# Kernel optimization log

Measured on AMD Instinct MI355X. Metric: run time of the kernel, lower is better.

Reference implementation:

```python
import jax, jax.numpy as jnp
import numpy as np

B, T, N, D = 64, 12, 512, 2      # batch, seq_len, num_nodes, input_dim
R, M, O, H = 64, 64, 1, 12       # rnn_units, message_size, output_dim, horizon


def setup_inputs() -> dict:
    key = jax.random.key(0)
    ks = jax.random.split(key, 12)
    inputs = jax.random.normal(ks[0], (B, T, N, D), jnp.float32)
    h0 = jax.random.normal(ks[1], (N, B, R), jnp.float32)  # torch.randn initial state
    adj = jax.random.uniform(ks[2], (N, N), jnp.float32)
    mask = jax.random.uniform(ks[3], (N, N)) < 0.05
    adj = jnp.where(mask, adj, 0.0)
    s = 1.0 / np.sqrt(R)
    u = lambda k, shape: jax.random.uniform(k, shape, jnp.float32, -s, s)
    return {
        "inputs": inputs, "h0": h0, "adj": adj,
        "W_msg": u(ks[4], (M, R)), "b_msg": u(ks[5], (M,)),
        "W_ih": u(ks[6], (3 * R, D + M)), "W_hh": u(ks[7], (3 * R, R)),
        "b_ih": u(ks[8], (3 * R,)), "b_hh": u(ks[9], (3 * R,)),
        "W_out": u(ks[10], (O * H, R)), "b_out": u(ks[11], (O * H,)),
    }


def reference(inputs, h0, adj, W_msg, b_msg, W_ih, W_hh, b_ih, b_hh, W_out, b_out):
    # mask matches the 'adj[j,i] > 0' guard in the python double loop
    adj_pos = jnp.where(adj > 0.0, adj, 0.0)

    def step(h, x_t):
        # h: [N, B, R]; x_t: [B, N, D]
        hw = h @ W_msg.T + b_msg                       # M_t(h): [N, B, M]
        # m[i] = sum_j adj[j, i] * hw[j]  -> dense masked aggregation
        m = jnp.einsum('ji,jbm->ibm', adj_pos, hw)     # [N, B, M]
        inp2 = jnp.concatenate([m, jnp.transpose(x_t, (1, 0, 2))], axis=2)  # [N, B, M+D]
        # torch GRUCell math (elementwise over the N*B 'batch'):
        gi = inp2 @ W_ih.T + b_ih                      # [N, B, 3R]
        gh = h @ W_hh.T + b_hh                         # [N, B, 3R]
        i_r, i_z, i_n = jnp.split(gi, 3, axis=-1)
        h_r, h_z, h_n = jnp.split(gh, 3, axis=-1)
        r = jax.nn.sigmoid(i_r + h_r)
        z = jax.nn.sigmoid(i_z + h_z)
        n = jnp.tanh(i_n + r * h_n)
        h_new = (1.0 - z) * n + z * h
        return h_new, None

    xs = jnp.transpose(inputs, (1, 0, 2, 3))           # [T, B, N, D]
    h, _ = jax.lax.scan(step, h0, xs)                  # [N, B, R]
    out = h @ W_out.T + b_out                          # R_t(h): [N, B, O*H]
    out = out.reshape(N, B, H, O)                      # reshape(N, B, horizon, -1)
    return jnp.transpose(out, (1, 2, 0, 3))            # [B, H, N, O]
```

## Files before the change

### kernel.cpp

```cpp
#include <hip/hip_runtime.h>

#define Bb 64
#define Tt 12
#define Nn 512
#define Dd 2
#define G3 192
#define Hh 12
#define CSR_CAP 96

typedef float f32x4 __attribute__((ext_vector_type(4)));
typedef _Float16 f16;
typedef _Float16 f16x8 __attribute__((ext_vector_type(8)));
typedef unsigned int uint_t;

__device__ __forceinline__ int swz4(int row, int bo) {
  return row * 256 + (bo ^ ((row & 7) << 4));
}

__global__ __launch_bounds__(256) void init_kernel(
    const float* __restrict__ h0, const float* __restrict__ adj,
    const float* __restrict__ W_msg, const float* __restrict__ W_ih,
    const float* __restrict__ W_hh, const float* __restrict__ b_ih,
    const float* __restrict__ b_hh, const float* __restrict__ b_msg,
    float* __restrict__ h_ws, f16* __restrict__ g_w, f16* __restrict__ g_wlo,
    float* __restrict__ g_f, int* __restrict__ g_cj,
    float* __restrict__ g_ca, int* __restrict__ g_nnz) {
  __shared__ int s_wavecnt[4];
  const int n = blockIdx.x, tid = threadIdx.x, l = tid & 63, wt = tid >> 6;

  {
    const int j0 = tid * 2, j1 = j0 + 1;
    const float a0 = adj[j0 * Nn + n];
    const float a1 = adj[j1 * Nn + n];
    unsigned long long mk0 = __ballot(a0 > 0.f);
    unsigned long long mk1 = __ballot(a1 > 0.f);
    if (l == 0) s_wavecnt[wt] = __popcll(mk0) + __popcll(mk1);
    __syncthreads();
    int base = 0;
#pragma unroll
    for (int w = 0; w < 4; ++w)
      if (w < wt) base += s_wavecnt[w];
    unsigned long long lt = (1ull << l) - 1ull;
    int pos = base + __popcll(mk0 & lt) + __popcll(mk1 & lt);
    if (a0 > 0.f) {
      if (pos < CSR_CAP) { g_cj[n * CSR_CAP + pos] = j0; g_ca[n * CSR_CAP + pos] = a0; }
      ++pos;
    }
    if (a1 > 0.f && pos < CSR_CAP) { g_cj[n * CSR_CAP + pos] = j1; g_ca[n * CSR_CAP + pos] = a1; }
    if (tid == 0) {
      int tot = s_wavecnt[0] + s_wavecnt[1] + s_wavecnt[2] + s_wavecnt[3];
      g_nnz[n] = tot < CSR_CAP ? tot : CSR_CAP;
    }
  }

  if (n == 0) {
    for (int tile = wt; tile < 24; tile += 4) {
      const int nt = tile >> 1, kt = tile & 1;
      const int wrow = nt * 16 + (l & 15);
      const int kc = kt * 32 + ((l >> 4) << 3);
      const float* s2 = W_ih + wrow * 66 + kc;
      const float* s1 = W_hh + wrow * 64 + kc;
#pragma unroll
      for (int j = 0; j < 8; ++j) {
        const float w2 = s2[j];
        const f16 h2 = (f16)w2;
        g_w[tile * 512 + l * 8 + j] = h2;
        g_wlo[tile * 512 + l * 8 + j] = (f16)(w2 - (float)h2);
        const float w1 = s1[j];
        const f16 h1 = (f16)w1;
        g_w[12288 + tile * 512 + l * 8 + j] = h1;
        g_wlo[12288 + tile * 512 + l * 8 + j] = (f16)(w1 - (float)h1);
      }
    }
    for (int tile = wt; tile < 8; tile += 4) {
      const int nt = tile >> 1, kt = tile & 1;
      const int wrow = nt * 16 + (l & 15);
      const int kc = kt * 32 + ((l >> 4) << 3);
      const float* s1 = W_msg + wrow * 64 + kc;
#pragma unroll
      for (int j = 0; j < 8; ++j) g_w[24576 + tile * 512 + l * 8 + j] = (f16)s1[j];
    }
    if (tid < G3) {
      g_f[tid * 2] = W_ih[tid * 66 + 64];
      g_f[tid * 2 + 1] = W_ih[tid * 66 + 65];
      g_f[384 + tid] = b_ih[tid];
      g_f[576 + tid] = b_hh[tid];
    }
    if (tid < 64) g_f[768 + tid] = b_msg[tid];
  }

  const float4* src = (const float4*)(h0 + ((size_t)n << 12));
  float4* dst = (float4*)(h_ws + ((size_t)n << 12));
  for (int i = tid; i < 1024; i += 256) dst[i] = src[i];
}

__global__ __launch_bounds__(256) void hw0_kernel(
    const float* __restrict__ h0, const f16* __restrict__ g_w,
    const float* __restrict__ g_f, f16* __restrict__ hw_out) {
  __shared__ float h_lds[4096];
  const int n = blockIdx.x, tid = threadIdx.x, l = tid & 63, wt = tid >> 6;
  {
    const int row = tid >> 2, c0 = (tid & 3) << 4;
    const float4* src = (const float4*)(h0 + ((n << 6) + row) * 64 + c0);
#pragma unroll
    for (int q = 0; q < 4; ++q)
      *(float4*)((char*)h_lds + swz4(row, c0 * 4 + q * 16)) = src[q];
  }
  const int ar = wt * 16 + (l & 15);
  const int bo = (l >> 4) << 5;
  float4 p0 = *(const float4*)((const char*)h_lds + swz4(ar, bo));
  float4 p1 = *(const float4*)((const char*)h_lds + swz4(ar, bo + 16));
  float4 p2 = *(const float4*)((const char*)h_lds + swz4(ar, 128 + bo));
  float4 p3 = *(const float4*)((const char*)h_lds + swz4(ar, 128 + bo + 16));
  f16x8 ahi0, alo0, ahi1, alo1;
  {
    float v[16] = {p0.x, p0.y, p0.z, p0.w, p1.x, p1.y, p1.z, p1.w,
                   p2.x, p2.y, p2.z, p2.w, p3.x, p3.y, p3.z, p3.w};
#pragma unroll
    for (int j = 0; j < 8; ++j) {
      f16 h = (f16)v[j];          ahi0[j] = h; alo0[j] = (f16)(v[j] - (float)h);
      f16 g = (f16)v[8 + j];      ahi1[j] = g; alo1[j] = (f16)(v[8 + j] - (float)g);
    }
  }
#pragma unroll
  for (int nt = 0; nt < 4; ++nt) {
    const f16x8 b0 = *(const f16x8*)(g_w + 24576 + (nt * 2 + 0) * 512 + l * 8);
    const f16x8 b1 = *(const f16x8*)(g_w + 24576 + (nt * 2 + 1) * 512 + l * 8);
    f32x4 c = {0.f, 0.f, 0.f, 0.f};
    c = __builtin_amdgcn_mfma_f32_16x16x32_f16(ahi0, b0, c, 0, 0, 0);
    c = __builtin_amdgcn_mfma_f32_16x16x32_f16(alo0, b0, c, 0, 0, 0);
    c = __builtin_amdgcn_mfma_f32_16x16x32_f16(ahi1, b1, c, 0, 0, 0);
    c = __builtin_amdgcn_mfma_f32_16x16x32_f16(alo1, b1, c, 0, 0, 0);
    const int col = nt * 16 + (l & 15);
    const float bm = g_f[768 + col];
#pragma unroll
    for (int g = 0; g < 4; ++g) {
      const int row = wt * 16 + ((l >> 4) << 2) + g;
      hw_out[((n << 6) + row) * 64 + col] = (f16)(c[g] + bm);
    }
  }
}

__global__ __launch_bounds__(256, 2) void step_kernel(
    const float* __restrict__ xin, float* __restrict__ h_ws,
    const uint4* __restrict__ g_blob, const f16* __restrict__ g_wlo,
    const int* __restrict__ g_cj, const float* __restrict__ g_ca,
    const int* __restrict__ g_nnz, const f16* __restrict__ hw_rd,
    f16* __restrict__ hw_wr, int t) {
  __shared__ uint4 sBlob[3792];
  __shared__ float h_lds[4096];
  __shared__ int s_cj[CSR_CAP];
  __shared__ float s_ca[CSR_CAP];
  const f16* sBih = (const f16*)sBlob;
  const f16* sBhh = sBih + 12288;
  const f16* sBmsg = sBih + 24576;
  const float* sF = (const float*)(sBih + 28672);
  const float* sWx = sF;
  const float* s_bih = sF + 384;
  const float* s_bhh = sF + 576;
  const float* s_bmsg = sF + 768;

  const int n = blockIdx.x, tid = threadIdx.x, l = tid & 63, wt = tid >> 6;

  for (int i = tid; i < 3792; i += 256) sBlob[i] = g_blob[i];
  if (tid < CSR_CAP) {
    s_cj[tid] = g_cj[n * CSR_CAP + tid];
    s_ca[tid] = g_ca[n * CSR_CAP + tid];
  }
  const int nnz = g_nnz[n];

  {
    const int row = tid >> 2, c0 = (tid & 3) << 4;
    const float4* src = (const float4*)(h_ws + ((n << 6) + row) * 64 + c0);
#pragma unroll
    for (int q = 0; q < 4; ++q)
      *(float4*)((char*)h_lds + swz4(row, c0 * 4 + q * 16)) = src[q];
  }
  float hreg[4][4];
#pragma unroll
  for (int ct = 0; ct < 4; ++ct)
#pragma unroll
    for (int g = 0; g < 4; ++g) {
      const int row = wt * 16 + ((l >> 4) << 2) + g;
      hreg[ct][g] = h_ws[((n << 6) + row) * 64 + ct * 16 + (l & 15)];
    }
  __syncthreads();

  const int mb = wt * 16 + (l & 15);
  const int mc0 = (l >> 4) << 3;
  float accm[16];
#pragma unroll
  for (int e = 0; e < 16; ++e) accm[e] = 0.f;
  for (int k = 0; k < nnz; ++k) {
    const int j = s_cj[k];
    const float a = s_ca[k];
    const f16* base = hw_rd + ((j << 6) + mb) * 64 + mc0;
    const f16x8 v0 = *(const f16x8*)(base);
    const f16x8 v1 = *(const f16x8*)(base + 32);
#pragma unroll
    for (int jj = 0; jj < 8; ++jj) {
      accm[jj] += a * (float)v0[jj];
      accm[8 + jj] += a * (float)v1[jj];
    }
  }
  f16x8 mhi0, mlo0, mhi1, mlo1;
#pragma unroll
  for (int jj = 0; jj < 8; ++jj) {
    f16 h = (f16)accm[jj];       mhi0[jj] = h; mlo0[jj] = (f16)(accm[jj] - (float)h);
    f16 g = (f16)accm[8 + jj];   mhi1[jj] = g; mlo1[jj] = (f16)(accm[8 + jj] - (float)g);
  }

  const int ar = wt * 16 + (l & 15);
  const int bo = (l >> 4) << 5;
  f16x8 ahi0, alo0, ahi1, alo1;
  {
    float4 p0 = *(const float4*)((const char*)h_lds + swz4(ar, bo));
    float4 p1 = *(const float4*)((const char*)h_lds + swz4(ar, bo + 16));
    float4 p2 = *(const float4*)((const char*)h_lds + swz4(ar, 128 + bo));
    float4 p3 = *(const float4*)((const char*)h_lds + swz4(ar, 128 + bo + 16));
    float v[16] = {p0.x, p0.y, p0.z, p0.w, p1.x, p1.y, p1.z, p1.w,
                   p2.x, p2.y, p2.z, p2.w, p3.x, p3.y, p3.z, p3.w};
#pragma unroll
    for (int j = 0; j < 8; ++j) {
      f16 h = (f16)v[j];        ahi0[j] = h; alo0[j] = (f16)(v[j] - (float)h);
      f16 g = (f16)v[8 + j];    ahi1[j] = g; alo1[j] = (f16)(v[8 + j] - (float)g);
    }
  }

  f32x4 cgi[12], cgh[12];
#pragma unroll
  for (int nt = 0; nt < 12; ++nt) {
    cgi[nt] = {0.f, 0.f, 0.f, 0.f};
    cgh[nt] = {0.f, 0.f, 0.f, 0.f};
  }
#pragma unroll
  for (int nt = 0; nt < 12; ++nt) {
    const f16x8 bh0 = *(const f16x8*)(sBhh + (nt * 2 + 0) * 512 + l * 8);
    const f16x8 bh1 = *(const f16x8*)(sBhh + (nt * 2 + 1) * 512 + l * 8);
    const f16x8 bhL0 = *(const f16x8*)(g_wlo + 12288 + (nt * 2 + 0) * 512 + l * 8);
    const f16x8 bhL1 = *(const f16x8*)(g_wlo + 12288 + (nt * 2 + 1) * 512 + l * 8);
    cgh[nt] = __builtin_amdgcn_mfma_f32_16x16x32_f16(ahi0, bh0, cgh[nt], 0, 0, 0);
    cgh[nt] = __builtin_amdgcn_mfma_f32_16x16x32_f16(alo0, bh0, cgh[nt], 0, 0, 0);
    cgh[nt] = __builtin_amdgcn_mfma_f32_16x16x32_f16(ahi1, bh1, cgh[nt], 0, 0, 0);
    cgh[nt] = __builtin_amdgcn_mfma_f32_16x16x32_f16(alo1, bh1, cgh[nt], 0, 0, 0);
    cgh[nt] = __builtin_amdgcn_mfma_f32_16x16x32_f16(ahi0, bhL0, cgh[nt], 0, 0, 0);
    cgh[nt] = __builtin_amdgcn_mfma_f32_16x16x32_f16(ahi1, bhL1, cgh[nt], 0, 0, 0);
    const f16x8 bi0 = *(const f16x8*)(sBih + (nt * 2 + 0) * 512 + l * 8);
    const f16x8 bi1 = *(const f16x8*)(sBih + (nt * 2 + 1) * 512 + l * 8);
    const f16x8 biL0 = *(const f16x8*)(g_wlo + (nt * 2 + 0) * 512 + l * 8);
    const f16x8 biL1 = *(const f16x8*)(g_wlo + (nt * 2 + 1) * 512 + l * 8);
    cgi[nt] = __builtin_amdgcn_mfma_f32_16x16x32_f16(mhi0, bi0, cgi[nt], 0, 0, 0);
    cgi[nt] = __builtin_amdgcn_mfma_f32_16x16x32_f16(mlo0, bi0, cgi[nt], 0, 0, 0);
    cgi[nt] = __builtin_amdgcn_mfma_f32_16x16x32_f16(mhi1, bi1, cgi[nt], 0, 0, 0);
    cgi[nt] = __builtin_amdgcn_mfma_f32_16x16x32_f16(mlo1, bi1, cgi[nt], 0, 0, 0);
    cgi[nt] = __builtin_amdgcn_mfma_f32_16x16x32_f16(mhi0, biL0, cgi[nt], 0, 0, 0);
    cgi[nt] = __builtin_amdgcn_mfma_f32_16x16x32_f16(mhi1, biL1, cgi[nt], 0, 0, 0);
  }

  float x0[4], x1[4];
#pragma unroll
  for (int g = 0; g < 4; ++g) {
    const int brow = wt * 16 + ((l >> 4) << 2) + g;
    const float* xp = xin + ((brow * Tt + t) * Nn + n) * Dd;
    x0[g] = xp[0];
    x1[g] = xp[1];
  }
#pragma unroll
  for (int ct = 0; ct < 4; ++ct) {
    const int colr = ct * 16 + (l & 15);
    const float wr0 = sWx[colr * 2], wr1 = sWx[colr * 2 + 1];
    const float wz0 = sWx[(colr + 64) * 2], wz1 = sWx[(colr + 64) * 2 + 1];
    const float wn0 = sWx[(colr + 128) * 2], wn1 = sWx[(colr + 128) * 2 + 1];
    const float bir = s_bih[colr], biz = s_bih[colr + 64], bin_ = s_bih[colr + 128];
    const float bhr = s_bhh[colr], bhz = s_bhh[colr + 64], bhn = s_bhh[colr + 128];
#pragma unroll
    for (int g = 0; g < 4; ++g) {
      const int row = wt * 16 + ((l >> 4) << 2) + g;
      const float gir = cgi[ct][g] + x0[g] * wr0 + x1[g] * wr1 + bir;
      const float giz = cgi[ct + 4][g] + x0[g] * wz0 + x1[g] * wz1 + biz;
      const float gin = cgi[ct + 8][g] + x0[g] * wn0 + x1[g] * wn1 + bin_;
      const float ghr = cgh[ct][g] + bhr;
      const float ghz = cgh[ct + 4][g] + bhz;
      const float ghn = cgh[ct + 8][g] + bhn;
      const float rg = 1.f / (1.f + __expf(-(gir + ghr)));
      const float zg = 1.f / (1.f + __expf(-(giz + ghz)));
      const float pa = gin + rg * ghn;
      const float e2 = __expf(-2.f * fabsf(pa));
      float th = (1.f - e2) / (1.f + e2);
      th = copysignf(th, pa);
      const float hn = (1.f - zg) * th + zg * hreg[ct][g];
      h_ws[((n << 6) + row) * 64 + colr] = hn;
      *(float*)((char*)h_lds + swz4(row, colr * 4)) = hn;
    }
  }

  if (t < Tt - 1) {
    f16x8 nhi0, nlo0, nhi1, nlo1;
    {
      float4 p0 = *(const float4*)((const char*)h_lds + swz4(ar, bo));
      float4 p1 = *(const float4*)((const char*)h_lds + swz4(ar, bo + 16));
      float4 p2 = *(const float4*)((const char*)h_lds + swz4(ar, 128 + bo));
      float4 p3 = *(const float4*)((const char*)h_lds + swz4(ar, 128 + bo + 16));
      float v[16] = {p0.x, p0.y, p0.z, p0.w, p1.x, p1.y, p1.z, p1.w,
                     p2.x, p2.y, p2.z, p2.w, p3.x, p3.y, p3.z, p3.w};
#pragma unroll
      for (int j = 0; j < 8; ++j) {
        f16 h = (f16)v[j];        nhi0[j] = h; nlo0[j] = (f16)(v[j] - (float)h);
        f16 g = (f16)v[8 + j];    nhi1[j] = g; nlo1[j] = (f16)(v[8 + j] - (float)g);
      }
    }
#pragma unroll
    for (int nt = 0; nt < 4; ++nt) {
      const f16x8 b0 = *(const f16x8*)(sBmsg + (nt * 2 + 0) * 512 + l * 8);
      const f16x8 b1 = *(const f16x8*)(sBmsg + (nt * 2 + 1) * 512 + l * 8);
      f32x4 c = {0.f, 0.f, 0.f, 0.f};
      c = __builtin_amdgcn_mfma_f32_16x16x32_f16(nhi0, b0, c, 0, 0, 0);
      c = __builtin_amdgcn_mfma_f32_16x16x32_f16(nlo0, b0, c, 0, 0, 0);
      c = __builtin_amdgcn_mfma_f32_16x16x32_f16(nhi1, b1, c, 0, 0, 0);
      c = __builtin_amdgcn_mfma_f32_16x16x32_f16(nlo1, b1, c, 0, 0, 0);
      const int col = nt * 16 + (l & 15);
      const float bm = s_bmsg[col];
#pragma unroll
      for (int g = 0; g < 4; ++g) {
        const int row = wt * 16 + ((l >> 4) << 2) + g;
        hw_wr[((n << 6) + row) * 64 + col] = (f16)(c[g] + bm);
      }
    }
  }
}

__global__ __launch_bounds__(256) void out_kernel(
    const float* __restrict__ h_ws, const float* __restrict__ W_out,
    const float* __restrict__ b_out, float* __restrict__ out) {
  __shared__ float sWo[Hh * 64];
  __shared__ float sbo[Hh];
  const int n = blockIdx.x, tid = threadIdx.x;
  for (int i = tid; i < Hh * 64; i += 256) sWo[i] = W_out[i];
  if (tid < Hh) sbo[tid] = b_out[tid];
  __syncthreads();
  for (int q = tid; q < Bb * Hh; q += 256) {
    const int b = q / Hh;
    const int o = q - b * Hh;
    const float* hr = h_ws + ((n << 6) + b) * 64;
    const float* wr = sWo + o * 64;
    float acc = sbo[o];
#pragma unroll 8
    for (int k = 0; k < 64; ++k) acc += hr[k] * wr[k];
    out[(b * Hh + o) * Nn + n] = acc;
  }
}

extern "C" void kernel_launch(void* const* d_in, const int* in_sizes, int n_in,
                              void* d_out, int out_size, void* d_ws, size_t ws_size,
                              hipStream_t stream) {
  const float* xin = (const float*)d_in[0];
  const float* h0 = (const float*)d_in[1];
  const float* adj = (const float*)d_in[2];
  const float* W_msg = (const float*)d_in[3];
  const float* b_msg = (const float*)d_in[4];
  const float* W_ih = (const float*)d_in[5];
  const float* W_hh = (const float*)d_in[6];
  const float* b_ih = (const float*)d_in[7];
  const float* b_hh = (const float*)d_in[8];
  const float* W_out = (const float*)d_in[9];
  const float* b_out = (const float*)d_in[10];
  float* out = (float*)d_out;

  char* ws = (char*)d_ws;
  float* h_ws = (float*)ws;
  f16* hwA = (f16*)(ws + (8u << 20));
  f16* hwB = (f16*)(ws + (12u << 20));
  char* base16 = ws + (16u << 20);
  f16* g_w = (f16*)base16;
  float* g_f = (float*)(base16 + 57344);
  f16* g_wlo = (f16*)(base16 + 61440);
  int* g_cj = (int*)(base16 + 110592);
  float* g_ca = (float*)(base16 + 110592 + 196608);
  int* g_nnz = (int*)(base16 + 110592 + 393216);
  const uint4* g_blob = (const uint4*)g_w;

  init_kernel<<<Nn, 256, 0, stream>>>(h0, adj, W_msg, W_ih, W_hh, b_ih, b_hh,
                                      b_msg, h_ws, g_w, g_wlo, g_f, g_cj, g_ca,
                                      g_nnz);
  hw0_kernel<<<Nn, 256, 0, stream>>>(h0, g_w, g_f, hwA);
  for (int t = 0; t < Tt; ++t) {
    f16* rd = (t & 1) ? hwB : hwA;
    f16* wr = (t & 1) ? hwA : hwB;
    step_kernel<<<Nn, 256, 0, stream>>>(xin, h_ws, g_blob, g_wlo, g_cj, g_ca,
                                        g_nnz, rd, wr, t);
  }
  out_kernel<<<Nn, 256, 0, stream>>>(h_ws, W_out, b_out, out);
}
```

Before: 469.7 us.

## Fuse output projection into last step, drop weight lo-splits, store hw in fp32

Several changes at once. The lo-part correction MFMAs on the GRU weights are removed, roughly halving matrix work per step. The message buffer hw moves from fp16 to fp32 and the gather is unrolled by two with float4 loads. The first step reads h0 directly instead of copying it, and the output projection is folded into the final step with an MFMA, which removes one launch. It also moves the CSR reads out of LDS and zero-pads the CSR. The risks are lower GRU-weight precision and twice the gather traffic from fp32 hw.

```diff
diff --git a/kernel.cpp b/kernel.cpp
--- a/kernel.cpp
+++ b/kernel.cpp
@@ -11,22 +11,25 @@
 typedef float f32x4 __attribute__((ext_vector_type(4)));
 typedef _Float16 f16;
 typedef _Float16 f16x8 __attribute__((ext_vector_type(8)));
-typedef unsigned int uint_t;
 
 __device__ __forceinline__ int swz4(int row, int bo) {
   return row * 256 + (bo ^ ((row & 7) << 4));
 }
 
 __global__ __launch_bounds__(256) void init_kernel(
-    const float* __restrict__ h0, const float* __restrict__ adj,
-    const float* __restrict__ W_msg, const float* __restrict__ W_ih,
-    const float* __restrict__ W_hh, const float* __restrict__ b_ih,
-    const float* __restrict__ b_hh, const float* __restrict__ b_msg,
-    float* __restrict__ h_ws, f16* __restrict__ g_w, f16* __restrict__ g_wlo,
+    const float* __restrict__ adj, const float* __restrict__ W_msg,
+    const float* __restrict__ W_ih, const float* __restrict__ W_hh,
+    const float* __restrict__ b_ih, const float* __restrict__ b_hh,
+    const float* __restrict__ b_msg, f16* __restrict__ g_w,
     float* __restrict__ g_f, int* __restrict__ g_cj,
     float* __restrict__ g_ca, int* __restrict__ g_nnz) {
   __shared__ int s_wavecnt[4];
   const int n = blockIdx.x, tid = threadIdx.x, l = tid & 63, wt = tid >> 6;
+
+  if (tid < CSR_CAP) {
+    g_cj[n * CSR_CAP + tid] = 0;
+    g_ca[n * CSR_CAP + tid] = 0.f;
+  }
 
   {
     const int j0 = tid * 2, j1 = j0 + 1;
@@ -62,14 +65,8 @@
       const float* s1 = W_hh + wrow * 64 + kc;
 #pragma unroll
       for (int j = 0; j < 8; ++j) {
-        const float w2 = s2[j];
-        const f16 h2 = (f16)w2;
-        g_w[tile * 512 + l * 8 + j] = h2;
-        g_wlo[tile * 512 + l * 8 + j] = (f16)(w2 - (float)h2);
-        const float w1 = s1[j];
-        const f16 h1 = (f16)w1;
-        g_w[12288 + tile * 512 + l * 8 + j] = h1;
-        g_wlo[12288 + tile * 512 + l * 8 + j] = (f16)(w1 - (float)h1);
+        g_w[tile * 512 + l * 8 + j] = (f16)s2[j];
+        g_w[12288 + tile * 512 + l * 8 + j] = (f16)s1[j];
       }
     }
     for (int tile = wt; tile < 8; tile += 4) {
@@ -88,15 +85,11 @@
     }
     if (tid < 64) g_f[768 + tid] = b_msg[tid];
   }
-
-  const float4* src = (const float4*)(h0 + ((size_t)n << 12));
-  float4* dst = (float4*)(h_ws + ((size_t)n << 12));
-  for (int i = tid; i < 1024; i += 256) dst[i] = src[i];
 }
 
 __global__ __launch_bounds__(256) void hw0_kernel(
     const float* __restrict__ h0, const f16* __restrict__ g_w,
-    const float* __restrict__ g_f, f16* __restrict__ hw_out) {
+    const float* __restrict__ g_f, float* __restrict__ hw_out) {
   __shared__ float h_lds[4096];
   const int n = blockIdx.x, tid = threadIdx.x, l = tid & 63, wt = tid >> 6;
   {
@@ -108,18 +101,18 @@
   }
   const int ar = wt * 16 + (l & 15);
   const int bo = (l >> 4) << 5;
-  float4 p0 = *(const float4*)((const char*)h_lds + swz4(ar, bo));
-  float4 p1 = *(const float4*)((const char*)h_lds + swz4(ar, bo + 16));
-  float4 p2 = *(const float4*)((const char*)h_lds + swz4(ar, 128 + bo));
-  float4 p3 = *(const float4*)((const char*)h_lds + swz4(ar, 128 + bo + 16));
   f16x8 ahi0, alo0, ahi1, alo1;
   {
+    float4 p0 = *(const float4*)((const char*)h_lds + swz4(ar, bo));
+    float4 p1 = *(const float4*)((const char*)h_lds + swz4(ar, bo + 16));
+    float4 p2 = *(const float4*)((const char*)h_lds + swz4(ar, 128 + bo));
+    float4 p3 = *(const float4*)((const char*)h_lds + swz4(ar, 128 + bo + 16));
     float v[16] = {p0.x, p0.y, p0.z, p0.w, p1.x, p1.y, p1.z, p1.w,
                    p2.x, p2.y, p2.z, p2.w, p3.x, p3.y, p3.z, p3.w};
 #pragma unroll
     for (int j = 0; j < 8; ++j) {
-      f16 h = (f16)v[j];          ahi0[j] = h; alo0[j] = (f16)(v[j] - (float)h);
-      f16 g = (f16)v[8 + j];      ahi1[j] = g; alo1[j] = (f16)(v[8 + j] - (float)g);
+      f16 h = (f16)v[j];        ahi0[j] = h; alo0[j] = (f16)(v[j] - (float)h);
+      f16 g = (f16)v[8 + j];    ahi1[j] = g; alo1[j] = (f16)(v[8 + j] - (float)g);
     }
   }
 #pragma unroll
@@ -136,21 +129,20 @@
 #pragma unroll
     for (int g = 0; g < 4; ++g) {
       const int row = wt * 16 + ((l >> 4) << 2) + g;
-      hw_out[((n << 6) + row) * 64 + col] = (f16)(c[g] + bm);
+      hw_out[((n << 6) + row) * 64 + col] = c[g] + bm;
     }
   }
 }
 
 __global__ __launch_bounds__(256, 2) void step_kernel(
-    const float* __restrict__ xin, float* __restrict__ h_ws,
-    const uint4* __restrict__ g_blob, const f16* __restrict__ g_wlo,
+    const float* __restrict__ xin, const float* __restrict__ h_src,
+    float* __restrict__ h_ws, const uint4* __restrict__ g_blob,
     const int* __restrict__ g_cj, const float* __restrict__ g_ca,
-    const int* __restrict__ g_nnz, const f16* __restrict__ hw_rd,
-    f16* __restrict__ hw_wr, int t) {
-  __shared__ uint4 sBlob[3792];
+    const int* __restrict__ g_nnz, const float* __restrict__ hw_rd,
+    float* __restrict__ hw_wr, const float* __restrict__ W_out,
+    const float* __restrict__ b_out, float* __restrict__ out, int t) {
+  __shared__ uint4 sBlob[3840];
   __shared__ float h_lds[4096];
-  __shared__ int s_cj[CSR_CAP];
-  __shared__ float s_ca[CSR_CAP];
   const f16* sBih = (const f16*)sBlob;
   const f16* sBhh = sBih + 12288;
   const f16* sBmsg = sBih + 24576;
@@ -162,53 +154,61 @@
 
   const int n = blockIdx.x, tid = threadIdx.x, l = tid & 63, wt = tid >> 6;
 
-  for (int i = tid; i < 3792; i += 256) sBlob[i] = g_blob[i];
-  if (tid < CSR_CAP) {
-    s_cj[tid] = g_cj[n * CSR_CAP + tid];
-    s_ca[tid] = g_ca[n * CSR_CAP + tid];
-  }
-  const int nnz = g_nnz[n];
-
+  float x0[4], x1[4];
+#pragma unroll
+  for (int g = 0; g < 4; ++g) {
+    const int brow = wt * 16 + ((l >> 4) << 2) + g;
+    const float2 xv = *(const float2*)(xin + ((brow * Tt + t) * Nn + n) * Dd);
+    x0[g] = xv.x; x1[g] = xv.y;
+  }
+  float hreg[4][4];
+#pragma unroll
+  for (int ct = 0; ct < 4; ++ct)
+#pragma unroll
+    for (int g = 0; g < 4; ++g) {
+      const int row = wt * 16 + ((l >> 4) << 2) + g;
+      hreg[ct][g] = h_src[((n << 6) + row) * 64 + ct * 16 + (l & 15)];
+    }
   {
     const int row = tid >> 2, c0 = (tid & 3) << 4;
-    const float4* src = (const float4*)(h_ws + ((n << 6) + row) * 64 + c0);
+    const float4* src = (const float4*)(h_src + ((n << 6) + row) * 64 + c0);
 #pragma unroll
     for (int q = 0; q < 4; ++q)
       *(float4*)((char*)h_lds + swz4(row, c0 * 4 + q * 16)) = src[q];
   }
-  float hreg[4][4];
-#pragma unroll
-  for (int ct = 0; ct < 4; ++ct)
-#pragma unroll
-    for (int g = 0; g < 4; ++g) {
-      const int row = wt * 16 + ((l >> 4) << 2) + g;
-      hreg[ct][g] = h_ws[((n << 6) + row) * 64 + ct * 16 + (l & 15)];
-    }
-  __syncthreads();
+  for (int i = tid; i < 3840; i += 256) sBlob[i] = g_blob[i];
 
   const int mb = wt * 16 + (l & 15);
   const int mc0 = (l >> 4) << 3;
+  const float* hwbase = hw_rd + mb * 64 + mc0;
   float accm[16];
 #pragma unroll
   for (int e = 0; e < 16; ++e) accm[e] = 0.f;
-  for (int k = 0; k < nnz; ++k) {
-    const int j = s_cj[k];
-    const float a = s_ca[k];
-    const f16* base = hw_rd + ((j << 6) + mb) * 64 + mc0;
-    const f16x8 v0 = *(const f16x8*)(base);
-    const f16x8 v1 = *(const f16x8*)(base + 32);
-#pragma unroll
-    for (int jj = 0; jj < 8; ++jj) {
-      accm[jj] += a * (float)v0[jj];
-      accm[8 + jj] += a * (float)v1[jj];
-    }
+  const int nnz = g_nnz[n];
+  for (int k = 0; k < nnz; k += 2) {
+    const int2 j2 = *(const int2*)(g_cj + n * CSR_CAP + k);
+    const float2 a2 = *(const float2*)(g_ca + n * CSR_CAP + k);
+    const float4* p0 = (const float4*)(hwbase + ((size_t)j2.x << 12));
+    const float4* p1 = (const float4*)(hwbase + ((size_t)j2.y << 12));
+    const float4 u0 = p0[0], u1 = p0[1], u2 = p0[8], u3 = p0[9];
+    const float4 v0 = p1[0], v1 = p1[1], v2 = p1[8], v3 = p1[9];
+    const float ax = a2.x, ay = a2.y;
+    accm[0] += ax * u0.x + ay * v0.x;  accm[1] += ax * u0.y + ay * v0.y;
+    accm[2] += ax * u0.z + ay * v0.z;  accm[3] += ax * u0.w + ay * v0.w;
+    accm[4] += ax * u1.x + ay * v1.x;  accm[5] += ax * u1.y + ay * v1.y;
+    accm[6] += ax * u1.z + ay * v1.z;  accm[7] += ax * u1.w + ay * v1.w;
+    accm[8] += ax * u2.x + ay * v2.x;  accm[9] += ax * u2.y + ay * v2.y;
+    accm[10] += ax * u2.z + ay * v2.z; accm[11] += ax * u2.w + ay * v2.w;
+    accm[12] += ax * u3.x + ay * v3.x; accm[13] += ax * u3.y + ay * v3.y;
+    accm[14] += ax * u3.z + ay * v3.z; accm[15] += ax * u3.w + ay * v3.w;
   }
   f16x8 mhi0, mlo0, mhi1, mlo1;
 #pragma unroll
-  for (int jj = 0; jj < 8; ++jj) {
-    f16 h = (f16)accm[jj];       mhi0[jj] = h; mlo0[jj] = (f16)(accm[jj] - (float)h);
-    f16 g = (f16)accm[8 + jj];   mhi1[jj] = g; mlo1[jj] = (f16)(accm[8 + jj] - (float)g);
-  }
+  for (int j = 0; j < 8; ++j) {
+    f16 h = (f16)accm[j];      mhi0[j] = h; mlo0[j] = (f16)(accm[j] - (float)h);
+    f16 g = (f16)accm[8 + j];  mhi1[j] = g; mlo1[j] = (f16)(accm[8 + j] - (float)g);
+  }
+  __syncthreads();
 
   const int ar = wt * 16 + (l & 15);
   const int bo = (l >> 4) << 5;
@@ -237,34 +237,18 @@
   for (int nt = 0; nt < 12; ++nt) {
     const f16x8 bh0 = *(const f16x8*)(sBhh + (nt * 2 + 0) * 512 + l * 8);
     const f16x8 bh1 = *(const f16x8*)(sBhh + (nt * 2 + 1) * 512 + l * 8);
-    const f16x8 bhL0 = *(const f16x8*)(g_wlo + 12288 + (nt * 2 + 0) * 512 + l * 8);
-    const f16x8 bhL1 = *(const f16x8*)(g_wlo + 12288 + (nt * 2 + 1) * 512 + l * 8);
     cgh[nt] = __builtin_amdgcn_mfma_f32_16x16x32_f16(ahi0, bh0, cgh[nt], 0, 0, 0);
     cgh[nt] = __builtin_amdgcn_mfma_f32_16x16x32_f16(alo0, bh0, cgh[nt], 0, 0, 0);
     cgh[nt] = __builtin_amdgcn_mfma_f32_16x16x32_f16(ahi1, bh1, cgh[nt], 0, 0, 0);
     cgh[nt] = __builtin_amdgcn_mfma_f32_16x16x32_f16(alo1, bh1, cgh[nt], 0, 0, 0);
-    cgh[nt] = __builtin_amdgcn_mfma_f32_16x16x32_f16(ahi0, bhL0, cgh[nt], 0, 0, 0);
-    cgh[nt] = __builtin_amdgcn_mfma_f32_16x16x32_f16(ahi1, bhL1, cgh[nt], 0, 0, 0);
     const f16x8 bi0 = *(const f16x8*)(sBih + (nt * 2 + 0) * 512 + l * 8);
     const f16x8 bi1 = *(const f16x8*)(sBih + (nt * 2 + 1) * 512 + l * 8);
-    const f16x8 biL0 = *(const f16x8*)(g_wlo + (nt * 2 + 0) * 512 + l * 8);
-    const f16x8 biL1 = *(const f16x8*)(g_wlo + (nt * 2 + 1) * 512 + l * 8);
     cgi[nt] = __builtin_amdgcn_mfma_f32_16x16x32_f16(mhi0, bi0, cgi[nt], 0, 0, 0);
     cgi[nt] = __builtin_amdgcn_mfma_f32_16x16x32_f16(mlo0, bi0, cgi[nt], 0, 0, 0);
     cgi[nt] = __builtin_amdgcn_mfma_f32_16x16x32_f16(mhi1, bi1, cgi[nt], 0, 0, 0);
     cgi[nt] = __builtin_amdgcn_mfma_f32_16x16x32_f16(mlo1, bi1, cgi[nt], 0, 0, 0);
-    cgi[nt] = __builtin_amdgcn_mfma_f32_16x16x32_f16(mhi0, biL0, cgi[nt], 0, 0, 0);
-    cgi[nt] = __builtin_amdgcn_mfma_f32_16x16x32_f16(mhi1, biL1, cgi[nt], 0, 0, 0);
-  }
-
-  float x0[4], x1[4];
-#pragma unroll
-  for (int g = 0; g < 4; ++g) {
-    const int brow = wt * 16 + ((l >> 4) << 2) + g;
-    const float* xp = xin + ((brow * Tt + t) * Nn + n) * Dd;
-    x0[g] = xp[0];
-    x1[g] = xp[1];
-  }
+  }
+
 #pragma unroll
   for (int ct = 0; ct < 4; ++ct) {
     const int colr = ct * 16 + (l & 15);
@@ -323,30 +307,47 @@
 #pragma unroll
       for (int g = 0; g < 4; ++g) {
         const int row = wt * 16 + ((l >> 4) << 2) + g;
-        hw_wr[((n << 6) + row) * 64 + col] = (f16)(c[g] + bm);
+        hw_wr[((n << 6) + row) * 64 + col] = c[g] + bm;
       }
     }
-  }
-}
-
-__global__ __launch_bounds__(256) void out_kernel(
-    const float* __restrict__ h_ws, const float* __restrict__ W_out,
-    const float* __restrict__ b_out, float* __restrict__ out) {
-  __shared__ float sWo[Hh * 64];
-  __shared__ float sbo[Hh];
-  const int n = blockIdx.x, tid = threadIdx.x;
-  for (int i = tid; i < Hh * 64; i += 256) sWo[i] = W_out[i];
-  if (tid < Hh) sbo[tid] = b_out[tid];
-  __syncthreads();
-  for (int q = tid; q < Bb * Hh; q += 256) {
-    const int b = q / Hh;
-    const int o = q - b * Hh;
-    const float* hr = h_ws + ((n << 6) + b) * 64;
-    const float* wr = sWo + o * 64;
-    float acc = sbo[o];
-#pragma unroll 8
-    for (int k = 0; k < 64; ++k) acc += hr[k] * wr[k];
-    out[(b * Hh + o) * Nn + n] = acc;
+  } else {
+    __syncthreads();
+    const int col = l & 15;
+    const int kc = (l >> 4) << 3;
+    f16x8 wo0 = {0, 0, 0, 0, 0, 0, 0, 0}, wo1 = {0, 0, 0, 0, 0, 0, 0, 0};
+    if (col < Hh) {
+      const float* wr_ = W_out + col * 64 + kc;
+      const float4 w0 = *(const float4*)(wr_);
+      const float4 w1 = *(const float4*)(wr_ + 4);
+      const float4 w2 = *(const float4*)(wr_ + 32);
+      const float4 w3 = *(const float4*)(wr_ + 36);
+      wo0[0] = (f16)w0.x; wo0[1] = (f16)w0.y; wo0[2] = (f16)w0.z; wo0[3] = (f16)w0.w;
+      wo0[4] = (f16)w1.x; wo0[5] = (f16)w1.y; wo0[6] = (f16)w1.z; wo0[7] = (f16)w1.w;
+      wo1[0] = (f16)w2.x; wo1[1] = (f16)w2.y; wo1[2] = (f16)w2.z; wo1[3] = (f16)w2.w;
+      wo1[4] = (f16)w3.x; wo1[5] = (f16)w3.y; wo1[6] = (f16)w3.z; wo1[7] = (f16)w3.w;
+    }
+    f16x8 hh0, hh1;
+    {
+      float4 p0 = *(const float4*)((const char*)h_lds + swz4(ar, bo));
+      float4 p1 = *(const float4*)((const char*)h_lds + swz4(ar, bo + 16));
+      float4 p2 = *(const float4*)((const char*)h_lds + swz4(ar, 128 + bo));
+      float4 p3 = *(const float4*)((const char*)h_lds + swz4(ar, 128 + bo + 16));
+      hh0[0] = (f16)p0.x; hh0[1] = (f16)p0.y; hh0[2] = (f16)p0.z; hh0[3] = (f16)p0.w;
+      hh0[4] = (f16)p1.x; hh0[5] = (f16)p1.y; hh0[6] = (f16)p1.z; hh0[7] = (f16)p1.w;
+      hh1[0] = (f16)p2.x; hh1[1] = (f16)p2.y; hh1[2] = (f16)p2.z; hh1[3] = (f16)p2.w;
+      hh1[4] = (f16)p3.x; hh1[5] = (f16)p3.y; hh1[6] = (f16)p3.z; hh1[7] = (f16)p3.w;
+    }
+    f32x4 c = {0.f, 0.f, 0.f, 0.f};
+    c = __builtin_amdgcn_mfma_f32_16x16x32_f16(hh0, wo0, c, 0, 0, 0);
+    c = __builtin_amdgcn_mfma_f32_16x16x32_f16(hh1, wo1, c, 0, 0, 0);
+    if (col < Hh) {
+      const float bo_ = b_out[col];
+#pragma unroll
+      for (int g = 0; g < 4; ++g) {
+        const int row = wt * 16 + ((l >> 4) << 2) + g;
+        out[(row * Hh + col) * Nn + n] = c[g] + bo_;
+      }
+    }
   }
 }
 
@@ -368,26 +369,24 @@
 
   char* ws = (char*)d_ws;
   float* h_ws = (float*)ws;
-  f16* hwA = (f16*)(ws + (8u << 20));
-  f16* hwB = (f16*)(ws + (12u << 20));
-  char* base16 = ws + (16u << 20);
-  f16* g_w = (f16*)base16;
-  float* g_f = (float*)(base16 + 57344);
-  f16* g_wlo = (f16*)(base16 + 61440);
-  int* g_cj = (int*)(base16 + 110592);
-  float* g_ca = (float*)(base16 + 110592 + 196608);
-  int* g_nnz = (int*)(base16 + 110592 + 393216);
-  const uint4* g_blob = (const uint4*)g_w;
-
-  init_kernel<<<Nn, 256, 0, stream>>>(h0, adj, W_msg, W_ih, W_hh, b_ih, b_hh,
-                                      b_msg, h_ws, g_w, g_wlo, g_f, g_cj, g_ca,
-                                      g_nnz);
+  float* hwA = (float*)(ws + (8u << 20));
+  float* hwB = (float*)(ws + (16u << 20));
+  char* base = ws + (24u << 20);
+  f16* g_w = (f16*)base;
+  float* g_f = (float*)(base + 57344);
+  int* g_cj = (int*)(base + 61440);
+  float* g_ca = (float*)(base + 61440 + 196608);
+  int* g_nnz = (int*)(base + 61440 + 393216);
+  const uint4* g_blob = (const uint4*)base;
+
+  init_kernel<<<Nn, 256, 0, stream>>>(adj, W_msg, W_ih, W_hh, b_ih, b_hh,
+                                      b_msg, g_w, g_f, g_cj, g_ca, g_nnz);
   hw0_kernel<<<Nn, 256, 0, stream>>>(h0, g_w, g_f, hwA);
   for (int t = 0; t < Tt; ++t) {
-    f16* rd = (t & 1) ? hwB : hwA;
-    f16* wr = (t & 1) ? hwA : hwB;
-    step_kernel<<<Nn, 256, 0, stream>>>(xin, h_ws, g_blob, g_wlo, g_cj, g_ca,
-                                        g_nnz, rd, wr, t);
-  }
-  out_kernel<<<Nn, 256, 0, stream>>>(h_ws, W_out, b_out, out);
-}
+    const float* rd = (t & 1) ? hwB : hwA;
+    float* wr = (t & 1) ? hwA : hwB;
+    const float* hs = (t == 0) ? h0 : h_ws;
+    step_kernel<<<Nn, 256, 0, stream>>>(xin, hs, h_ws, g_blob, g_cj, g_ca,
+                                        g_nnz, rd, wr, W_out, b_out, out, t);
+  }
+}
```

Result: slower. 615.2 us (+31.0%).
